# Optimization experiments

Measured on AMD Instinct MI355X. Metric: run time of the kernel, lower is better.

## Reference

```python
import jax, jax.numpy as jnp
import numpy as np

D_MODEL = 1024
N_HEADS = 16
HEAD_SIZE = D_MODEL // N_HEADS
D_FF = 4096
EPS = 1e-6


def _layernorm(x, g, b):
    # Faithful to source: (x + mean) / (std + eps), unbiased std (torch default)
    mean = jnp.mean(x, axis=-1, keepdims=True)
    std = jnp.std(x, axis=-1, keepdims=True, ddof=1)
    return g * ((x + mean) / (std + EPS)) + b


def setup_inputs() -> dict:
    key = jax.random.key(0)
    ks = jax.random.split(key, 12)
    s = lambda fan_in: 1.0 / np.sqrt(fan_in)
    x = jax.random.normal(ks[0], (4, 2048, D_MODEL), dtype=jnp.float32)
    Wq = jax.random.uniform(ks[1], (N_HEADS, D_MODEL, HEAD_SIZE), jnp.float32, -s(D_MODEL), s(D_MODEL))
    Wk = jax.random.uniform(ks[2], (N_HEADS, D_MODEL, HEAD_SIZE), jnp.float32, -s(D_MODEL), s(D_MODEL))
    Wv = jax.random.uniform(ks[3], (N_HEADS, D_MODEL, HEAD_SIZE), jnp.float32, -s(D_MODEL), s(D_MODEL))
    Wo = jax.random.uniform(ks[4], (D_MODEL, D_MODEL), jnp.float32, -s(D_MODEL), s(D_MODEL))
    bo = jax.random.uniform(ks[5], (D_MODEL,), jnp.float32, -s(D_MODEL), s(D_MODEL))
    W1 = jax.random.uniform(ks[6], (D_MODEL, D_FF), jnp.float32, -s(D_MODEL), s(D_MODEL))
    b1 = jax.random.uniform(ks[7], (D_FF,), jnp.float32, -s(D_MODEL), s(D_MODEL))
    W2 = jax.random.uniform(ks[8], (D_FF, D_MODEL), jnp.float32, -s(D_FF), s(D_FF))
    b2 = jax.random.uniform(ks[9], (D_MODEL,), jnp.float32, -s(D_FF), s(D_FF))
    g1 = jnp.ones((D_MODEL,), jnp.float32)
    be1 = jnp.zeros((D_MODEL,), jnp.float32)
    g2 = jnp.ones((D_MODEL,), jnp.float32)
    be2 = jnp.zeros((D_MODEL,), jnp.float32)
    return {"x": x, "Wq": Wq, "Wk": Wk, "Wv": Wv, "Wo": Wo, "bo": bo,
            "W1": W1, "b1": b1, "W2": W2, "b2": b2,
            "g1": g1, "be1": be1, "g2": g2, "be2": be2}


def reference(x, Wq, Wk, Wv, Wo, bo, W1, b1, W2, b2, g1, be1, g2, be2):
    # Multi-head attention; note: source scales by sqrt(d_model), not sqrt(head_size)
    scale = 1.0 / np.sqrt(D_MODEL)
    q = jnp.einsum('bsd,hde->bhse', x, Wq)
    k = jnp.einsum('bsd,hde->bhse', x, Wk)
    v = jnp.einsum('bsd,hde->bhse', x, Wv)
    scores = jnp.einsum('bhse,bhte->bhst', q, k) * scale
    attn = jax.nn.softmax(scores, axis=-1)
    o = jnp.einsum('bhst,bhte->bhse', attn, v)
    B, H, S, E = o.shape
    o = o.transpose(0, 2, 1, 3).reshape(B, S, H * E)  # concat heads
    mha_out = o @ Wo + bo

    h1 = _layernorm(x + mha_out, g1, be1)

    ff = jax.nn.relu(h1 @ W1 + b1) @ W2 + b2
    out = _layernorm(h1 + ff, g2, be2)
    return out
```

## Files before the change

kernel.cpp:

```cpp
#include <hip/hip_runtime.h>

typedef short short8 __attribute__((ext_vector_type(8)));
typedef short short4v __attribute__((ext_vector_type(4)));
typedef float floatx4 __attribute__((ext_vector_type(4)));

#define D_MODEL 1024
#define N_HEADS 16
#define HEAD    64
#define D_FF    4096
#define SEQ     2048
#define BATCH   4
#define TOKENS  (BATCH*SEQ)

__device__ __forceinline__ float b2f(unsigned short u) {
  return __uint_as_float(((unsigned)u) << 16);
}
__device__ __forceinline__ unsigned short f2b(float f) {
  unsigned u = __float_as_uint(f);
  unsigned r = 0x7fffu + ((u >> 16) & 1u);
  return (unsigned short)((u + r) >> 16);
}
__device__ __forceinline__ floatx4 mfma16(short8 a, short8 b, floatx4 c) {
  return __builtin_amdgcn_mfma_f32_16x16x32_bf16(a, b, c, 0, 0, 0);
}
__device__ __forceinline__ void load16_lds(const unsigned short* g, unsigned short* l) {
  __builtin_amdgcn_global_load_lds((const __attribute__((address_space(1))) void*)g,
                                   (__attribute__((address_space(3))) void*)l, 16, 0, 0);
}

__device__ __forceinline__ void transp_body(
    const float* __restrict__ src, unsigned short* __restrict__ dst,
    int R, int C, int bx, int by, float (*t)[65])
{
  int cb = bx * 64, rb = by * 64;
#pragma unroll
  for (int i = 0; i < 16; i++) {
    int idx = i * 256 + threadIdx.x;
    int lr = idx >> 6, lc = idx & 63;
    t[lr][lc] = src[(size_t)(rb + lr) * C + cb + lc];
  }
  __syncthreads();
#pragma unroll
  for (int i = 0; i < 16; i++) {
    int idx = i * 256 + threadIdx.x;
    int lc = idx >> 6, lr = idx & 63;
    dst[(size_t)(cb + lc) * R + rb + lr] = f2b(t[lr][lc]);
  }
}

__global__ __launch_bounds__(256) void prep_kernel(
    const float* __restrict__ x, unsigned short* __restrict__ x_bf,
    const float* __restrict__ Wq, const float* __restrict__ Wk,
    const float* __restrict__ Wv, unsigned short* __restrict__ qkv_bt,
    const float* __restrict__ Wo, unsigned short* __restrict__ wo_bt,
    const float* __restrict__ W1, unsigned short* __restrict__ w1_bt,
    const float* __restrict__ W2, unsigned short* __restrict__ w2_bt)
{
  __shared__ float t[64][65];
  int bid = blockIdx.x;
  if (bid < 8192) {
    int idx = bid * 1024 + threadIdx.x * 4;
    float4 v = *(const float4*)(x + idx);
    short4v o;
    o[0] = (short)f2b(v.x); o[1] = (short)f2b(v.y);
    o[2] = (short)f2b(v.z); o[3] = (short)f2b(v.w);
    *(short4v*)(x_bf + idx) = o;
  } else if (bid < 8960) {
    int by = bid - 8192;
    int xt = by & 15, z = by >> 4;
    int sel = z >> 4, h = z & 15;
    const float* W = (sel == 0) ? Wq : ((sel == 1) ? Wk : Wv);
    const float* src = W + (size_t)h * D_MODEL * HEAD;
    int rb = xt * 64;
#pragma unroll
    for (int i = 0; i < 16; i++) {
      int idx = i * 256 + threadIdx.x;
      int lr = idx >> 6, lc = idx & 63;
      t[lr][lc] = src[(size_t)(rb + lr) * HEAD + lc];
    }
    __syncthreads();
    unsigned short* d0 = qkv_bt + (size_t)(sel * 1024 + h * 64) * D_MODEL;
#pragma unroll
    for (int i = 0; i < 16; i++) {
      int idx = i * 256 + threadIdx.x;
      int lc = idx >> 6, lr = idx & 63;
      d0[(size_t)lc * D_MODEL + rb + lr] = f2b(t[lr][lc]);
    }
  } else if (bid < 9216) {
    int i = bid - 8960;
    transp_body(Wo, wo_bt, 1024, 1024, i & 15, i >> 4, t);
  } else if (bid < 10240) {
    int i = bid - 9216;
    transp_body(W1, w1_bt, 1024, 4096, i & 63, i >> 6, t);
  } else {
    int i = bid - 10240;
    transp_body(W2, w2_bt, 4096, 1024, i & 15, i >> 4, t);
  }
}

__global__ __launch_bounds__(512, 2) void gemm256(
    const unsigned short* __restrict__ A, const unsigned short* __restrict__ BT,
    const float* __restrict__ biasf, void* __restrict__ outp,
    int M, int N, int K, int epi)
{
  __shared__ unsigned short a_sh[2 * 256 * 64];
  __shared__ unsigned short b_sh[2 * 256 * 64];

  const int tid  = threadIdx.x;
  const int lane = tid & 63;
  const int wave = tid >> 6;
  const int quad = lane >> 4;
  const int l15  = lane & 15;
  const int wm   = wave >> 2;
  const int wn   = wave & 3;

  const int lin = blockIdx.y * gridDim.x + blockIdx.x;
  const int xcd = lin & 7, j = lin >> 3;
  const int m0 = (xcd * 4 + (j & 3)) * 256;
  const int n0 = (j >> 2) * 256;

  const int u  = tid >> 3;
  const int sc = (tid & 7) ^ (u & 7);
  const unsigned short* a_src = A  + (size_t)(m0 + u) * K + sc * 8;
  const int borig = ((u >> 5) * 64) + (u & 31);
  const unsigned short* b_src = BT + (size_t)(n0 + borig) * K + sc * 8;
  unsigned short* a_dst = a_sh + wave * 512;
  unsigned short* b_dst = b_sh + wave * 512;

#define SA(T, Rc)  load16_lds(a_src + (size_t)(Rc) * K + (T) * 64, \
                              a_dst + ((T) & 1) * 16384 + (Rc) * 64)
#define SB(T, Rb, Radd) load16_lds(b_src + (size_t)(Radd) * K + (T) * 64, \
                              b_dst + ((T) & 1) * 16384 + (Rb) * 64)
#define STG_A0(T) do { SA(T, 0);   SA(T, 128); } while (0)
#define STG_A1(T) do { SA(T, 64);  SA(T, 192); } while (0)
#define STG_B0(T) do { SB(T, 0, 0);    SB(T, 64, 128); } while (0)
#define STG_B1(T) do { SB(T, 128, 32); SB(T, 192, 160); } while (0)

  floatx4 acc[8][4] = {};
  short8 aF[4][2];
  short8 bF[2][2][2];
  const unsigned short* ash = a_sh;
  const unsigned short* bsh = b_sh;

#define LDA(QM) \
  _Pragma("unroll") for (int mi = 0; mi < 4; mi++) \
  _Pragma("unroll") for (int kh = 0; kh < 2; kh++) \
    aF[mi][kh] = *(const short8*)(ash + (wm * 128 + (QM) * 64 + mi * 16 + l15) * 64 \
                                  + (((kh * 4 + quad) ^ (l15 & 7)) * 8));
#define LDB(QN) \
  _Pragma("unroll") for (int ni = 0; ni < 2; ni++) \
  _Pragma("unroll") for (int kh = 0; kh < 2; kh++) \
    bF[QN][ni][kh] = *(const short8*)(bsh + ((QN) * 128 + wn * 32 + ni * 16 + l15) * 64 \
                                      + (((kh * 4 + quad) ^ (l15 & 7)) * 8));
#define MM(QM, QN) \
  _Pragma("unroll") for (int mi = 0; mi < 4; mi++) \
  _Pragma("unroll") for (int ni = 0; ni < 2; ni++) { \
    acc[(QM) * 4 + mi][(QN) * 2 + ni] = \
        mfma16(aF[mi][0], bF[QN][ni][0], acc[(QM) * 4 + mi][(QN) * 2 + ni]); \
    acc[(QM) * 4 + mi][(QN) * 2 + ni] = \
        mfma16(aF[mi][1], bF[QN][ni][1], acc[(QM) * 4 + mi][(QN) * 2 + ni]); \
  }
#define PH_VM(N) asm volatile("s_waitcnt vmcnt(" #N ")" ::: "memory");
#define PH_MID() \
  __builtin_amdgcn_s_barrier(); \
  asm volatile("s_waitcnt lgkmcnt(0)" ::: "memory"); \
  __builtin_amdgcn_sched_barrier(0); \
  __builtin_amdgcn_s_setprio(1);
#define PH_END() \
  __builtin_amdgcn_s_setprio(0); \
  __builtin_amdgcn_s_barrier();

  const int NT = K >> 6;

  STG_A0(0); STG_B0(0); STG_A1(0); STG_B1(0); STG_A0(1); STG_B0(1);
  PH_VM(4)
  __builtin_amdgcn_s_barrier();

  for (int t = 0; t < NT - 2; ++t) {
    ash = a_sh + (t & 1) * 16384;
    bsh = b_sh + (t & 1) * 16384;

    LDA(0) LDB(0)
    STG_A1(t + 1);
    PH_MID() MM(0, 0) PH_END();

    LDB(1)
    STG_B1(t + 1);
    PH_MID() MM(0, 1) PH_END();

    LDA(1)
    STG_A0(t + 2);
    PH_MID() MM(1, 0) PH_END();

    STG_B0(t + 2);
    PH_VM(4)
    PH_MID() MM(1, 1) PH_END();
  }
  {
    const int t = NT - 2;
    ash = a_sh + (t & 1) * 16384;
    bsh = b_sh + (t & 1) * 16384;

    LDA(0) LDB(0)
    STG_A1(t + 1);
    PH_MID() MM(0, 0) PH_END();

    LDB(1)
    STG_B1(t + 1);
    PH_MID() MM(0, 1) PH_END();

    LDA(1)
    PH_MID() MM(1, 0) PH_END();

    PH_VM(0)
    PH_MID() MM(1, 1) PH_END();
  }
  {
    const int t = NT - 1;
    ash = a_sh + (t & 1) * 16384;
    bsh = b_sh + (t & 1) * 16384;

    LDA(0) LDB(0)
    PH_MID() MM(0, 0) PH_END();

    LDB(1)
    PH_MID() MM(0, 1) PH_END();

    LDA(1)
    PH_MID() MM(1, 0) PH_END();

    PH_MID() MM(1, 1) PH_END();
  }

#undef SA
#undef SB
#undef STG_A0
#undef STG_A1
#undef STG_B0
#undef STG_B1
#undef LDA
#undef LDB
#undef MM
#undef PH_VM
#undef PH_MID
#undef PH_END

#pragma unroll
  for (int mi = 0; mi < 8; mi++) {
#pragma unroll
    for (int ni = 0; ni < 4; ni++) {
      const int col = n0 + wn * 64 + ni * 16 + l15;
      const int row0 = m0 + wm * 128 + mi * 16 + quad * 4;
      if (epi == 0) {
        int sel = col >> 10;
        int cc = col & 1023;
        int h = cc >> 6, e = cc & 63;
        int b = row0 >> 11, s0 = row0 & 2047;
        if (sel < 2) {
          unsigned short* base = (unsigned short*)outp + (size_t)sel * 8388608;
#pragma unroll
          for (int r = 0; r < 4; r++) {
            float v2 = (sel == 0) ? acc[mi][ni][r] * 0.04508422f : acc[mi][ni][r];
            base[((size_t)((b * N_HEADS + h) * SEQ + (s0 + r))) * HEAD + e] = f2b(v2);
          }
        } else {
          unsigned short* base = (unsigned short*)outp + (size_t)2 * 8388608;
          short4v pk;
#pragma unroll
          for (int r = 0; r < 4; r++) pk[r] = (short)f2b(acc[mi][ni][r]);
          *(short4v*)(base + ((size_t)((b * N_HEADS + h) * HEAD + e)) * SEQ + s0) = pk;
        }
      } else {
#pragma unroll
        for (int r = 0; r < 4; r++)
          ((unsigned short*)outp)[(size_t)(row0 + r) * N + col] =
              f2b(fmaxf(acc[mi][ni][r] + biasf[col], 0.0f));
      }
    }
  }
}

__global__ __launch_bounds__(512, 2) void gemm256n(
    const unsigned short* __restrict__ A, const unsigned short* __restrict__ BT,
    const float* __restrict__ biasf, const float* __restrict__ residf,
    const unsigned short* __restrict__ residb, void* __restrict__ outp,
    int M, int N, int K, int epi)
{
  __shared__ unsigned short a_sh[2 * 256 * 64];
  __shared__ unsigned short b_sh[2 * 128 * 64];

  const int tid  = threadIdx.x;
  const int lane = tid & 63;
  const int wave = tid >> 6;
  const int quad = lane >> 4;
  const int l15  = lane & 15;
  const int wm   = wave >> 1;
  const int wn   = wave & 1;

  const int lin = blockIdx.y * gridDim.x + blockIdx.x;
  const int xcd = lin & 7, j = lin >> 3;
  const int m0 = (xcd * 4 + (j & 3)) * 256;
  const int n0 = (j >> 2) * 128;

  const int u  = tid >> 3;
  const int sc = (tid & 7) ^ (u & 7);
  const unsigned short* a_src = A  + (size_t)(m0 + u) * K + sc * 8;
  const unsigned short* b_src = BT + (size_t)(n0 + u) * K + sc * 8;
  unsigned short* a_dst = a_sh + wave * 512;
  unsigned short* b_dst = b_sh + wave * 512;

#define SA(T, Rc) load16_lds(a_src + (size_t)(Rc) * K + (T) * 64, \
                             a_dst + ((T) & 1) * 16384 + (Rc) * 64)
#define SB(T, Rb) load16_lds(b_src + (size_t)(Rb) * K + (T) * 64, \
                             b_dst + ((T) & 1) * 8192 + (Rb) * 64)
#define STG_A0(T) do { SA(T, 0);   SA(T, 64);  } while (0)
#define STG_A1(T) do { SA(T, 128); SA(T, 192); } while (0)
#define STG_B(T)  do { SB(T, 0);   SB(T, 64);  } while (0)

  floatx4 acc[4][4] = {};
  short8 aF[2][2];
  short8 bF[2][2][2];
  const unsigned short* ash = a_sh;
  const unsigned short* bsh = b_sh;

#define LDA(QM) \
  _Pragma("unroll") for (int mi = 0; mi < 2; mi++) \
  _Pragma("unroll") for (int kh = 0; kh < 2; kh++) \
    aF[mi][kh] = *(const short8*)(ash + ((QM) * 128 + wm * 32 + mi * 16 + l15) * 64 \
                                  + (((kh * 4 + quad) ^ (l15 & 7)) * 8));
#define LDB(QN) \
  _Pragma("unroll") for (int ni = 0; ni < 2; ni++) \
  _Pragma("unroll") for (int kh = 0; kh < 2; kh++) \
    bF[QN][ni][kh] = *(const short8*)(bsh + ((QN) * 64 + wn * 32 + ni * 16 + l15) * 64 \
                                      + (((kh * 4 + quad) ^ (l15 & 7)) * 8));
#define MM2(QM) \
  _Pragma("unroll") for (int qn = 0; qn < 2; qn++) \
  _Pragma("unroll") for (int mi = 0; mi < 2; mi++) \
  _Pragma("unroll") for (int ni = 0; ni < 2; ni++) { \
    acc[(QM) * 2 + mi][qn * 2 + ni] = \
        mfma16(aF[mi][0], bF[qn][ni][0], acc[(QM) * 2 + mi][qn * 2 + ni]); \
    acc[(QM) * 2 + mi][qn * 2 + ni] = \
        mfma16(aF[mi][1], bF[qn][ni][1], acc[(QM) * 2 + mi][qn * 2 + ni]); \
  }
#define PH_VM(N) asm volatile("s_waitcnt vmcnt(" #N ")" ::: "memory");
#define PH_MID() \
  __builtin_amdgcn_s_barrier(); \
  asm volatile("s_waitcnt lgkmcnt(0)" ::: "memory"); \
  __builtin_amdgcn_sched_barrier(0); \
  __builtin_amdgcn_s_setprio(1);
#define PH_END() \
  __builtin_amdgcn_s_setprio(0); \
  __builtin_amdgcn_s_barrier();

  const int NT = K >> 6;

  STG_A0(0); STG_B(0); STG_A1(0); STG_A0(1); STG_B(1);
  PH_VM(4)
  __builtin_amdgcn_s_barrier();

  for (int t = 0; t < NT - 2; ++t) {
    ash = a_sh + (t & 1) * 16384;
    bsh = b_sh + (t & 1) * 8192;

    LDA(0) LDB(0) LDB(1)
    STG_A1(t + 1);
    PH_MID() MM2(0) PH_END();

    LDA(1)
    STG_A0(t + 2); STG_B(t + 2);
    PH_VM(4)
    PH_MID() MM2(1) PH_END();
  }
  {
    const int t = NT - 2;
    ash = a_sh + (t & 1) * 16384;
    bsh = b_sh + (t & 1) * 8192;

    LDA(0) LDB(0) LDB(1)
    STG_A1(t + 1);
    PH_MID() MM2(0) PH_END();

    LDA(1)
    PH_VM(0)
    PH_MID() MM2(1) PH_END();
  }
  {
    const int t = NT - 1;
    ash = a_sh + (t & 1) * 16384;
    bsh = b_sh + (t & 1) * 8192;

    LDA(0) LDB(0) LDB(1)
    PH_MID() MM2(0) PH_END();

    LDA(1)
    PH_MID() MM2(1) PH_END();
  }

#undef SA
#undef SB
#undef STG_A0
#undef STG_A1
#undef STG_B
#undef LDA
#undef LDB
#undef MM2
#undef PH_VM
#undef PH_MID
#undef PH_END

#pragma unroll
  for (int am = 0; am < 4; am++) {
    const int row0 = m0 + (am >> 1) * 128 + wm * 32 + (am & 1) * 16 + quad * 4;
#pragma unroll
    for (int bn = 0; bn < 4; bn++) {
      const int col = n0 + (bn >> 1) * 64 + wn * 32 + (bn & 1) * 16 + l15;
      if (epi == 1) {
#pragma unroll
        for (int r = 0; r < 4; r++)
          ((float*)outp)[(size_t)(row0 + r) * N + col] =
              acc[am][bn][r] + biasf[col] + residf[(size_t)(row0 + r) * N + col];
      } else {
#pragma unroll
        for (int r = 0; r < 4; r++)
          ((float*)outp)[(size_t)(row0 + r) * N + col] =
              acc[am][bn][r] + biasf[col] + b2f(residb[(size_t)(row0 + r) * N + col]);
      }
    }
  }
}

__global__ __launch_bounds__(256, 4) void attn_kernel(
    const unsigned short* __restrict__ q, const unsigned short* __restrict__ k,
    const unsigned short* __restrict__ vt, unsigned short* __restrict__ o)
{
  const int bh = blockIdx.y;
  const int qt = blockIdx.x;
  const int tid = threadIdx.x, lane = tid & 63, wave = tid >> 6;
  const int quad = lane >> 4, l15 = lane & 15;
  const size_t base = (size_t)bh * SEQ * HEAD;

  __shared__ unsigned short k_sh[64 * 64];
  __shared__ unsigned short vT_sh[64 * 64];
  __shared__ unsigned short p_sh[4 * 32 * 72];
  unsigned short* pw = p_sh + wave * 32 * 72;

  short8 qf[2][2];
#pragma unroll
  for (int mj = 0; mj < 2; mj++) {
    const unsigned short* qp =
        q + base + (size_t)(qt * 128 + wave * 32 + mj * 16 + l15) * HEAD;
    qf[mj][0] = *(const short8*)(qp + quad * 8);
    qf[mj][1] = *(const short8*)(qp + 32 + quad * 8);
  }

  floatx4 oacc[2][4] = {};
  floatx4 rsacc[2] = {};

  short8 onesf;
  {
    short ov = (l15 == 0) ? (short)0x3F80 : (short)0;
#pragma unroll
    for (int jj = 0; jj < 8; jj++) onesf[jj] = ov;
  }

  const int r8 = lane >> 3, slot = lane & 7;

  for (int kt = 0; kt < SEQ / 64; kt++) {
    __syncthreads();
#pragma unroll
    for (int i = 0; i < 2; i++) {
      int t = wave * 16 + i * 8 + r8;
      int cg = slot ^ (t & 7);
      load16_lds(k + base + (size_t)(kt * 64 + t) * HEAD + cg * 8,
                 k_sh + (wave * 16 + i * 8) * 64);
      load16_lds(vt + base + (size_t)t * SEQ + kt * 64 + cg * 8,
                 vT_sh + (wave * 16 + i * 8) * 64);
    }
    __syncthreads();

#pragma unroll
    for (int ti = 0; ti < 4; ti++) {
      int t = ti * 16 + l15;
      short8 kf0 = *(const short8*)(k_sh + t * 64 + ((quad ^ (t & 7)) * 8));
      short8 kf1 = *(const short8*)(k_sh + t * 64 + (((4 + quad) ^ (t & 7)) * 8));
      floatx4 s0 = {0.f, 0.f, 0.f, 0.f}, s1 = {0.f, 0.f, 0.f, 0.f};
      __builtin_amdgcn_s_setprio(1);
      s0 = mfma16(kf0, qf[0][0], s0);
      s0 = mfma16(kf1, qf[0][1], s0);
      s1 = mfma16(kf0, qf[1][0], s1);
      s1 = mfma16(kf1, qf[1][1], s1);
      __builtin_amdgcn_s_setprio(0);
#pragma unroll
      for (int mj = 0; mj < 2; mj++) {
        floatx4 s = mj ? s1 : s0;
        float p0 = __builtin_amdgcn_exp2f(s[0]);
        float p1 = __builtin_amdgcn_exp2f(s[1]);
        float p2 = __builtin_amdgcn_exp2f(s[2]);
        float p3 = __builtin_amdgcn_exp2f(s[3]);
        uint2 u;
        u.x = __builtin_amdgcn_perm(__float_as_uint(p1), __float_as_uint(p0), 0x07060302u);
        u.y = __builtin_amdgcn_perm(__float_as_uint(p3), __float_as_uint(p2), 0x07060302u);
        *(uint2*)(pw + (mj * 16 + l15) * 72 + ti * 16 + quad * 4) = u;
      }
    }

    {
      short8 pf[2][2];
#pragma unroll
      for (int mj = 0; mj < 2; mj++) {
        pf[mj][0] = *(const short8*)(pw + (mj * 16 + l15) * 72 + quad * 8);
        pf[mj][1] = *(const short8*)(pw + (mj * 16 + l15) * 72 + 32 + quad * 8);
      }
      __builtin_amdgcn_s_setprio(1);
#pragma unroll
      for (int ni = 0; ni < 4; ni++) {
        int e = ni * 16 + l15;
        short8 bv0 = *(const short8*)(vT_sh + e * 64 + ((quad ^ (e & 7)) * 8));
        short8 bv1 = *(const short8*)(vT_sh + e * 64 + (((4 + quad) ^ (e & 7)) * 8));
#pragma unroll
        for (int mj = 0; mj < 2; mj++) {
          oacc[mj][ni] = mfma16(pf[mj][0], bv0, oacc[mj][ni]);
          oacc[mj][ni] = mfma16(pf[mj][1], bv1, oacc[mj][ni]);
        }
      }
#pragma unroll
      for (int mj = 0; mj < 2; mj++) {
        rsacc[mj] = mfma16(pf[mj][0], onesf, rsacc[mj]);
        rsacc[mj] = mfma16(pf[mj][1], onesf, rsacc[mj]);
      }
      __builtin_amdgcn_s_setprio(0);
    }
  }

  const int b = bh >> 4, h = bh & 15;
#pragma unroll
  for (int mj = 0; mj < 2; mj++)
#pragma unroll
    for (int r = 0; r < 4; r++) {
      int s = qt * 128 + wave * 32 + mj * 16 + quad * 4 + r;
      float rsv = __shfl(rsacc[mj][r], quad * 16, 64);
      float inv = 1.0f / rsv;
#pragma unroll
      for (int ni = 0; ni < 4; ni++)
        o[((size_t)(b * SEQ + s)) * D_MODEL + h * HEAD + ni * 16 + l15] =
            f2b(oacc[mj][ni][r] * inv);
    }
}

__global__ __launch_bounds__(256) void ln_kernel(
    const float* __restrict__ in, const float* __restrict__ g,
    const float* __restrict__ be, void* __restrict__ outp, int write_bf16)
{
  const int row = blockIdx.x * 4 + (threadIdx.x >> 6);
  const int lane = threadIdx.x & 63;
  const float* xp = in + (size_t)row * D_MODEL;
  float4 xv[4];
  float s = 0.0f, ss = 0.0f;
#pragma unroll
  for (int j = 0; j < 4; j++) {
    xv[j] = *(const float4*)(xp + j * 256 + lane * 4);
    s += (xv[j].x + xv[j].y) + (xv[j].z + xv[j].w);
    ss += (xv[j].x * xv[j].x + xv[j].y * xv[j].y) +
          (xv[j].z * xv[j].z + xv[j].w * xv[j].w);
  }
#pragma unroll
  for (int m = 1; m < 64; m <<= 1) {
    s += __shfl_xor(s, m, 64);
    ss += __shfl_xor(ss, m, 64);
  }
  float mean = s * (1.0f / 1024.0f);
  float var = fmaxf((ss - 1024.0f * mean * mean) * (1.0f / 1023.0f), 0.0f);
  float inv = 1.0f / (sqrtf(var) + 1e-6f);
#pragma unroll
  for (int j = 0; j < 4; j++) {
    int c = j * 256 + lane * 4;
    float4 g4 = *(const float4*)(g + c);
    float4 b4 = *(const float4*)(be + c);
    float y0 = g4.x * ((xv[j].x + mean) * inv) + b4.x;
    float y1 = g4.y * ((xv[j].y + mean) * inv) + b4.y;
    float y2 = g4.z * ((xv[j].z + mean) * inv) + b4.z;
    float y3 = g4.w * ((xv[j].w + mean) * inv) + b4.w;
    if (write_bf16) {
      short4v o4;
      o4[0] = (short)f2b(y0); o4[1] = (short)f2b(y1);
      o4[2] = (short)f2b(y2); o4[3] = (short)f2b(y3);
      *(short4v*)((unsigned short*)outp + (size_t)row * D_MODEL + c) = o4;
    } else {
      float4 o4 = {y0, y1, y2, y3};
      *(float4*)((float*)outp + (size_t)row * D_MODEL + c) = o4;
    }
  }
}

extern "C" void kernel_launch(void* const* d_in, const int* in_sizes, int n_in,
                              void* d_out, int out_size, void* d_ws, size_t ws_size,
                              hipStream_t stream)
{
  const float* x   = (const float*)d_in[0];
  const float* Wq  = (const float*)d_in[1];
  const float* Wk  = (const float*)d_in[2];
  const float* Wv  = (const float*)d_in[3];
  const float* Wo  = (const float*)d_in[4];
  const float* bo  = (const float*)d_in[5];
  const float* W1  = (const float*)d_in[6];
  const float* b1  = (const float*)d_in[7];
  const float* W2  = (const float*)d_in[8];
  const float* b2  = (const float*)d_in[9];
  const float* g1  = (const float*)d_in[10];
  const float* be1 = (const float*)d_in[11];
  const float* g2  = (const float*)d_in[12];
  const float* be2 = (const float*)d_in[13];
  float* out = (float*)d_out;

  unsigned short* ws     = (unsigned short*)d_ws;
  unsigned short* w1_bt  = ws;
  unsigned short* w2_bt  = ws + 4194304;
  unsigned short* qkv_bt = ws + 8388608;
  unsigned short* wo_bt  = ws + 11534336;
  unsigned short* x_bf   = ws + 12582912;
  unsigned short* qws    = ws + 20971520;
  unsigned short* kws    = ws + 29360128;
  unsigned short* vws    = ws + 37748736;
  unsigned short* ows    = x_bf;
  float*          r1     = (float*)(ws + 20971520);
  unsigned short* h1_bf  = x_bf;
  unsigned short* ff1    = ws + 20971520;

  dim3 blk(256);

  prep_kernel<<<11264, blk, 0, stream>>>(x, x_bf, Wq, Wk, Wv, qkv_bt,
                                         Wo, wo_bt, W1, w1_bt, W2, w2_bt);

  gemm256<<<dim3(3072 / 256, TOKENS / 256), dim3(512), 0, stream>>>(
      x_bf, qkv_bt, nullptr, qws, TOKENS, 3072, 1024, 0);
  attn_kernel<<<dim3(SEQ / 128, BATCH * N_HEADS), blk, 0, stream>>>(qws, kws, vws, ows);
  gemm256n<<<dim3(1024 / 128, TOKENS / 256), dim3(512), 0, stream>>>(
      ows, wo_bt, bo, x, nullptr, r1, TOKENS, 1024, 1024, 1);
  ln_kernel<<<TOKENS / 4, blk, 0, stream>>>(r1, g1, be1, h1_bf, 1);
  gemm256<<<dim3(4096 / 256, TOKENS / 256), dim3(512), 0, stream>>>(
      h1_bf, w1_bt, b1, ff1, TOKENS, 4096, 1024, 2);
  gemm256n<<<dim3(1024 / 128, TOKENS / 256), dim3(512), 0, stream>>>(
      ff1, w2_bt, b2, nullptr, h1_bf, out, TOKENS, 1024, 4096, 3);
  ln_kernel<<<TOKENS / 4, blk, 0, stream>>>(out, g2, be2, out, 0);
}
```

Baseline: 470.8 us.

## Double-buffer K/V tiles in attention kernel to overlap loads with compute

The attention kernel now keeps two LDS buffers for the K and V^T tiles. It issues the asynchronous global-to-LDS load for the next key tile before computing on the current one, which cuts the per-iteration barrier count from two to one. The aim is to hide global memory latency behind the MFMA and exp work. In exchange LDS use per block roughly doubles for K/V, and the launch-bounds occupancy hint of 4 blocks per CU is dropped, which may lower occupancy or change register allocation.

```diff
diff --git a/kernel.cpp b/kernel.cpp
--- a/kernel.cpp
+++ b/kernel.cpp
@@ -429,7 +429,7 @@
   }
 }
 
-__global__ __launch_bounds__(256, 4) void attn_kernel(
+__global__ __launch_bounds__(256) void attn_kernel(
     const unsigned short* __restrict__ q, const unsigned short* __restrict__ k,
     const unsigned short* __restrict__ vt, unsigned short* __restrict__ o)
 {
@@ -439,8 +439,8 @@
   const int quad = lane >> 4, l15 = lane & 15;
   const size_t base = (size_t)bh * SEQ * HEAD;
 
-  __shared__ unsigned short k_sh[64 * 64];
-  __shared__ unsigned short vT_sh[64 * 64];
+  __shared__ unsigned short k_sh[2 * 4096];
+  __shared__ unsigned short vT_sh[2 * 4096];
   __shared__ unsigned short p_sh[4 * 32 * 72];
   unsigned short* pw = p_sh + wave * 32 * 72;
 
@@ -465,24 +465,31 @@
 
   const int r8 = lane >> 3, slot = lane & 7;
 
+#define STAGE(B, KT) do { \
+    _Pragma("unroll") \
+    for (int i_ = 0; i_ < 2; i_++) { \
+      int t_ = wave * 16 + i_ * 8 + r8; \
+      int cg_ = slot ^ (t_ & 7); \
+      load16_lds(k + base + (size_t)((KT) * 64 + t_) * HEAD + cg_ * 8, \
+                 k_sh + (B) * 4096 + (wave * 16 + i_ * 8) * 64); \
+      load16_lds(vt + base + (size_t)t_ * SEQ + (KT) * 64 + cg_ * 8, \
+                 vT_sh + (B) * 4096 + (wave * 16 + i_ * 8) * 64); \
+    } } while (0)
+
+  STAGE(0, 0);
+  __syncthreads();
+
   for (int kt = 0; kt < SEQ / 64; kt++) {
-    __syncthreads();
-#pragma unroll
-    for (int i = 0; i < 2; i++) {
-      int t = wave * 16 + i * 8 + r8;
-      int cg = slot ^ (t & 7);
-      load16_lds(k + base + (size_t)(kt * 64 + t) * HEAD + cg * 8,
-                 k_sh + (wave * 16 + i * 8) * 64);
-      load16_lds(vt + base + (size_t)t * SEQ + kt * 64 + cg * 8,
-                 vT_sh + (wave * 16 + i * 8) * 64);
-    }
-    __syncthreads();
+    const int cur = kt & 1;
+    if (kt + 1 < SEQ / 64) STAGE(cur ^ 1, kt + 1);
+    const unsigned short* ks = k_sh + cur * 4096;
+    const unsigned short* vs = vT_sh + cur * 4096;
 
 #pragma unroll
     for (int ti = 0; ti < 4; ti++) {
       int t = ti * 16 + l15;
-      short8 kf0 = *(const short8*)(k_sh + t * 64 + ((quad ^ (t & 7)) * 8));
-      short8 kf1 = *(const short8*)(k_sh + t * 64 + (((4 + quad) ^ (t & 7)) * 8));
+      short8 kf0 = *(const short8*)(ks + t * 64 + ((quad ^ (t & 7)) * 8));
+      short8 kf1 = *(const short8*)(ks + t * 64 + (((4 + quad) ^ (t & 7)) * 8));
       floatx4 s0 = {0.f, 0.f, 0.f, 0.f}, s1 = {0.f, 0.f, 0.f, 0.f};
       __builtin_amdgcn_s_setprio(1);
       s0 = mfma16(kf0, qf[0][0], s0);
@@ -515,8 +522,8 @@
 #pragma unroll
       for (int ni = 0; ni < 4; ni++) {
         int e = ni * 16 + l15;
-        short8 bv0 = *(const short8*)(vT_sh + e * 64 + ((quad ^ (e & 7)) * 8));
-        short8 bv1 = *(const short8*)(vT_sh + e * 64 + (((4 + quad) ^ (e & 7)) * 8));
+        short8 bv0 = *(const short8*)(vs + e * 64 + ((quad ^ (e & 7)) * 8));
+        short8 bv1 = *(const short8*)(vs + e * 64 + (((4 + quad) ^ (e & 7)) * 8));
 #pragma unroll
         for (int mj = 0; mj < 2; mj++) {
           oacc[mj][ni] = mfma16(pf[mj][0], bv0, oacc[mj][ni]);
@@ -530,7 +537,10 @@
       }
       __builtin_amdgcn_s_setprio(0);
     }
-  }
+
+    __syncthreads();
+  }
+#undef STAGE
 
   const int b = bh >> 4, h = bh & 15;
 #pragma unroll
```

Result: slower. 511.5 us (+8.7%).

## Load attention K/V fragments directly from global memory with XCD-aware block mapping

Applied to the files above, without the earlier changes.

Removes the shared-memory staging of K and V tiles and the two block barriers per key tile, so each wave reads its MFMA operands straight from global memory and relies on L2/L1 caching. Remaps the linear block index so that all query tiles of one (batch, head) land on the same XCD, which should improve L2 reuse of that head's K/V. Raises the occupancy hint from 4 to 6 blocks per CU, which the lower LDS use makes possible. In exchange, every wave now issues redundant global loads of the same K/V data and waits on global-memory latency without explicit prefetching.

```diff
diff --git a/kernel.cpp b/kernel.cpp
--- a/kernel.cpp
+++ b/kernel.cpp
@@ -429,18 +429,19 @@
   }
 }
 
-__global__ __launch_bounds__(256, 4) void attn_kernel(
+__global__ __launch_bounds__(256, 6) void attn_kernel(
     const unsigned short* __restrict__ q, const unsigned short* __restrict__ k,
     const unsigned short* __restrict__ vt, unsigned short* __restrict__ o)
 {
-  const int bh = blockIdx.y;
-  const int qt = blockIdx.x;
+  const int lin = blockIdx.y * gridDim.x + blockIdx.x;
+  const int xcd = lin & 7, g = lin >> 3;
+  const int qt = g & 15;
+  const int bh = (g >> 4) * 8 + xcd;
+
   const int tid = threadIdx.x, lane = tid & 63, wave = tid >> 6;
   const int quad = lane >> 4, l15 = lane & 15;
   const size_t base = (size_t)bh * SEQ * HEAD;
 
-  __shared__ unsigned short k_sh[64 * 64];
-  __shared__ unsigned short vT_sh[64 * 64];
   __shared__ unsigned short p_sh[4 * 32 * 72];
   unsigned short* pw = p_sh + wave * 32 * 72;
 
@@ -463,26 +464,15 @@
     for (int jj = 0; jj < 8; jj++) onesf[jj] = ov;
   }
 
-  const int r8 = lane >> 3, slot = lane & 7;
-
   for (int kt = 0; kt < SEQ / 64; kt++) {
-    __syncthreads();
-#pragma unroll
-    for (int i = 0; i < 2; i++) {
-      int t = wave * 16 + i * 8 + r8;
-      int cg = slot ^ (t & 7);
-      load16_lds(k + base + (size_t)(kt * 64 + t) * HEAD + cg * 8,
-                 k_sh + (wave * 16 + i * 8) * 64);
-      load16_lds(vt + base + (size_t)t * SEQ + kt * 64 + cg * 8,
-                 vT_sh + (wave * 16 + i * 8) * 64);
-    }
-    __syncthreads();
+    const unsigned short* kb = k + base + (size_t)kt * 64 * HEAD;
+    const unsigned short* vb = vt + base + (size_t)kt * 64;
 
 #pragma unroll
     for (int ti = 0; ti < 4; ti++) {
       int t = ti * 16 + l15;
-      short8 kf0 = *(const short8*)(k_sh + t * 64 + ((quad ^ (t & 7)) * 8));
-      short8 kf1 = *(const short8*)(k_sh + t * 64 + (((4 + quad) ^ (t & 7)) * 8));
+      short8 kf0 = *(const short8*)(kb + (size_t)t * HEAD + quad * 8);
+      short8 kf1 = *(const short8*)(kb + (size_t)t * HEAD + 32 + quad * 8);
       floatx4 s0 = {0.f, 0.f, 0.f, 0.f}, s1 = {0.f, 0.f, 0.f, 0.f};
       __builtin_amdgcn_s_setprio(1);
       s0 = mfma16(kf0, qf[0][0], s0);
@@ -515,8 +505,8 @@
 #pragma unroll
       for (int ni = 0; ni < 4; ni++) {
         int e = ni * 16 + l15;
-        short8 bv0 = *(const short8*)(vT_sh + e * 64 + ((quad ^ (e & 7)) * 8));
-        short8 bv1 = *(const short8*)(vT_sh + e * 64 + (((4 + quad) ^ (e & 7)) * 8));
+        short8 bv0 = *(const short8*)(vb + (size_t)e * SEQ + quad * 8);
+        short8 bv1 = *(const short8*)(vb + (size_t)e * SEQ + 32 + quad * 8);
 #pragma unroll
         for (int mj = 0; mj < 2; mj++) {
           oacc[mj][ni] = mfma16(pf[mj][0], bv0, oacc[mj][ni]);
```

Result: slower. 709.3 us (+50.7%).
